# Performance work log

Hardware: AMD Instinct MI355X
Metric: run time of the kernel (lower is better)

Reference implementation:

```python
import jax, jax.numpy as jnp
import numpy as np

SIGMA = 1.0  # RBF kernel bandwidth (init kwarg)

def setup_inputs() -> dict:
    key = jax.random.key(0)
    ks = jax.random.split(key, 5)
    B, N, D_in, D_emb = 8, 2048, 1024, 512
    scale = 1.0 / np.sqrt(D_in)
    return {
        "x": jax.random.normal(ks[0], (B, N, D_in), jnp.float32),
        "W_mu": jax.random.normal(ks[1], (D_emb, D_in), jnp.float32) * scale,
        "b_mu": jax.random.normal(ks[2], (D_emb,), jnp.float32) * scale,
        "W_logvar": jax.random.normal(ks[3], (D_emb, D_in), jnp.float32) * scale,
        "b_logvar": jax.random.normal(ks[4], (D_emb,), jnp.float32) * scale,
    }

def reference(x, W_mu, b_mu, W_logvar, b_logvar):
    # dual linear heads: (B,N,D_in) -> (B,N,D_emb)
    mu = jnp.einsum('bnd,ed->bne', x, W_mu) + b_mu
    logvar = jnp.einsum('bnd,ed->bne', x, W_logvar) + b_logvar
    sigma = jnp.exp(0.5 * logvar)
    # RBF kernel matrix K(x, x): (B,N,N) via ||xi||^2 + ||xj||^2 - 2 xi.xj
    sq = jnp.sum(x * x, axis=-1)                       # (B,N)
    gram = jnp.einsum('bnd,bmd->bnm', x, x)            # (B,N,N)
    dist = sq[:, :, None] + sq[:, None, :] - 2.0 * gram
    K = jnp.exp(-dist / (2.0 * SIGMA ** 2))            # (B,N,N)
    cov_diag = jnp.diagonal(K, axis1=1, axis2=2)       # (B,N) == exp(0) = 1
    sigma_adjusted = sigma * cov_diag[..., None]       # (B,N,D_emb)
    return (mu, sigma_adjusted)
```

## Files before the change

kernel.cpp:

```cpp
#include <hip/hip_runtime.h>
#include <hip/hip_bf16.h>
#include <math.h>

typedef __bf16 bf16;
typedef __attribute__((ext_vector_type(4))) float f32x4;
typedef __attribute__((ext_vector_type(4))) bf16 bf16x4;
typedef __attribute__((ext_vector_type(8))) bf16 bf16x8;

#define M_TOT 16384
#define K_TOT 1024
#define D_EMB 512
#define NT 32

__global__ __launch_bounds__(256) void cvt_w_img(
    const float* __restrict__ W_mu, const float* __restrict__ W_logvar,
    bf16* __restrict__ img)
{
    const int c  = blockIdx.x * 256 + threadIdx.x;
    const int l  = c & 63;
    const int kt = (c >> 6) & 31;
    const int es = c >> 11;
    const int col = es * 16 + (l & 15);
    const int k0  = kt * 32 + (l >> 4) * 8;
    const float* s = (col < D_EMB) ? (W_mu + (size_t)col * K_TOT + k0)
                                   : (W_logvar + (size_t)(col - D_EMB) * K_TOT + k0);
    f32x4 a = ((const f32x4*)s)[0];
    f32x4 b = ((const f32x4*)s)[1];
    bf16x8 o;
    o[0] = (bf16)a[0]; o[1] = (bf16)a[1]; o[2] = (bf16)a[2]; o[3] = (bf16)a[3];
    o[4] = (bf16)b[0]; o[5] = (bf16)b[1]; o[6] = (bf16)b[2]; o[7] = (bf16)b[3];
    *(bf16x8*)(img + (size_t)c * 8) = o;
}

__global__ __launch_bounds__(512, 1) void gpe_tall(
    const float* __restrict__ x,
    const bf16* __restrict__ wimg,
    const float* __restrict__ b_mu,
    const float* __restrict__ b_logvar,
    float* __restrict__ out)
{
    __shared__ __align__(16) bf16 Alds[2][64 * 32];

    const int tid  = threadIdx.x;
    const int lane = tid & 63;
    const int wc   = tid >> 6;
    const int fr   = lane & 15;
    const int g16  = lane >> 4;
    const int bm   = blockIdx.x;

    const int arow = tid >> 3;
    const int aslot = tid & 7;
    const float* __restrict__ Asrc = x + (size_t)(bm * 64 + arow) * K_TOT + aslot * 4;
    const int awoff = arow * 32 + aslot * 4;

    const bf16* __restrict__ bb = wimg + (size_t)(wc * 8) * (NT * 512) + lane * 8;

    f32x4 acc[4][8];
#pragma unroll
    for (int m = 0; m < 4; ++m)
#pragma unroll
        for (int n = 0; n < 8; ++n)
            acc[m][n] = (f32x4){0.f, 0.f, 0.f, 0.f};

    f32x4  pfA;
    bf16x8 bvA[8], bvB[8];

    auto gloadA = [&](int t) { pfA = *(const f32x4*)(Asrc + t * 32); };
    auto cwA = [&](bf16* base) {
        bf16x4 w;
#pragma unroll
        for (int j = 0; j < 4; ++j) w[j] = (bf16)pfA[j];
        *(bf16x4*)&base[awoff] = w;
    };
    auto loadB = [&](int t, bf16x8 (&bv)[8]) {
#pragma unroll
        for (int ns = 0; ns < 8; ++ns)
            bv[ns] = *(const bf16x8*)(bb + (size_t)ns * (NT * 512) + t * 512);
    };

    gloadA(0);
    cwA(&Alds[0][0]);
    gloadA(1);
    loadB(0, bvA);
    asm volatile("s_waitcnt lgkmcnt(0)" ::: "memory");
    __builtin_amdgcn_s_barrier();

#define TILE_BODY(T, P, BVC, BVN)                                              \
    {                                                                          \
        const int t = (T);                                                     \
        if (t + 1 < NT) loadB(t + 1, BVN);                \
        bf16x8 afc[4];                                                         \
        _Pragma("unroll")                                                      \
        for (int m = 0; m < 4; ++m)                                            \
            afc[m] = *(const bf16x8*)&Alds[P][(m * 16 + fr) * 32 + g16 * 8];   \
        if (t + 1 < NT) {                                                      \
            cwA(&Alds[(P) ^ 1][0]);                   \
            if (t + 2 < NT) gloadA(t + 2);                                     \
        }                                                                      \
        __builtin_amdgcn_s_setprio(1);                                         \
        _Pragma("unroll")                                                      \
        for (int ns = 0; ns < 8; ++ns)                                         \
            _Pragma("unroll")                                                  \
            for (int m = 0; m < 4; ++m)                                        \
                acc[m][ns] = __builtin_amdgcn_mfma_f32_16x16x32_bf16(          \
                    afc[m], BVC[ns], acc[m][ns], 0, 0, 0);                     \
        __builtin_amdgcn_s_setprio(0);                                         \
        asm volatile("s_waitcnt lgkmcnt(0)" ::: "memory");                     \
        __builtin_amdgcn_s_barrier();                                          \
    }

    for (int t0 = 0; t0 < NT; t0 += 2) {
        TILE_BODY(t0,     0, bvA, bvB)
        TILE_BODY(t0 + 1, 1, bvB, bvA)
    }
#undef TILE_BODY

    const bool is_mu = (wc < 4);
    const float* __restrict__ bias = is_mu ? b_mu : b_logvar;
    float* __restrict__ obase = is_mu ? out : (out + (size_t)M_TOT * D_EMB);
    const int clbase = (wc & 3) * 128;

#pragma unroll
    for (int m = 0; m < 4; ++m) {
        const int row0 = bm * 64 + m * 16 + g16 * 4;
#pragma unroll
        for (int ns = 0; ns < 8; ++ns) {
            const int cl = clbase + ns * 16 + fr;
            const float bvs = bias[cl];
#pragma unroll
            for (int j = 0; j < 4; ++j) {
                float v = acc[m][ns][j] + bvs;
                if (!is_mu) v = __expf(0.5f * v);
                obase[(size_t)(row0 + j) * D_EMB + cl] = v;
            }
        }
    }
}

#define LDS_STRIDE 40
__global__ __launch_bounds__(256) void gpe_gemm_fb(
    const float* __restrict__ x, const float* __restrict__ W_mu,
    const float* __restrict__ b_mu, const float* __restrict__ W_logvar,
    const float* __restrict__ b_logvar, float* __restrict__ out)
{
    __shared__ __align__(16) bf16 As[128][LDS_STRIDE];
    __shared__ __align__(16) bf16 Bs[128][LDS_STRIDE];
    const int tid = threadIdx.x, lane = tid & 63, wid = tid >> 6;
    const int wr = wid >> 1, wcn = wid & 1;
    const int bn = blockIdx.x & 7, bm = blockIdx.x >> 3;
    const int ebase = bn * 128;
    const bool is_mu = (ebase < D_EMB);
    const float* Wp = is_mu ? (W_mu + (size_t)ebase * K_TOT)
                            : (W_logvar + (size_t)(ebase - D_EMB) * K_TOT);
    const float* bias = is_mu ? b_mu : b_logvar;
    const int cbase = is_mu ? ebase : (ebase - D_EMB);
    float* obase = is_mu ? out : (out + (size_t)M_TOT * D_EMB);
    const float* Ap = x + (size_t)(bm * 128) * K_TOT;
    f32x4 acc[4][4];
#pragma unroll
    for (int m = 0; m < 4; ++m)
#pragma unroll
        for (int n = 0; n < 4; ++n) acc[m][n] = (f32x4){0.f, 0.f, 0.f, 0.f};
    const int fr = lane & 15, fk = (lane >> 4) * 8;
    const int arow = wr * 64 + fr, brow = wcn * 64 + fr;
    for (int kt = 0; kt < K_TOT / 32; ++kt) {
        const int k0 = kt * 32;
#pragma unroll
        for (int s = 0; s < 4; ++s) {
            const int idx = s * 256 + tid;
            const int row = idx >> 3, col = (idx & 7) << 2;
            f32x4 va = *reinterpret_cast<const f32x4*>(Ap + (size_t)row * K_TOT + k0 + col);
            f32x4 vb = *reinterpret_cast<const f32x4*>(Wp + (size_t)row * K_TOT + k0 + col);
            bf16x4 ha, hb;
#pragma unroll
            for (int j = 0; j < 4; ++j) { ha[j] = (bf16)va[j]; hb[j] = (bf16)vb[j]; }
            *reinterpret_cast<bf16x4*>(&As[row][col]) = ha;
            *reinterpret_cast<bf16x4*>(&Bs[row][col]) = hb;
        }
        __syncthreads();
        bf16x8 af[4], bfv[4];
#pragma unroll
        for (int m = 0; m < 4; ++m)
            af[m] = *reinterpret_cast<const bf16x8*>(&As[arow + m * 16][fk]);
#pragma unroll
        for (int n = 0; n < 4; ++n)
            bfv[n] = *reinterpret_cast<const bf16x8*>(&Bs[brow + n * 16][fk]);
#pragma unroll
        for (int m = 0; m < 4; ++m)
#pragma unroll
            for (int n = 0; n < 4; ++n)
                acc[m][n] = __builtin_amdgcn_mfma_f32_16x16x32_bf16(af[m], bfv[n], acc[m][n], 0, 0, 0);
        __syncthreads();
    }
#pragma unroll
    for (int m = 0; m < 4; ++m) {
        const int rbase = bm * 128 + wr * 64 + m * 16 + (lane >> 4) * 4;
#pragma unroll
        for (int n = 0; n < 4; ++n) {
            const int c = cbase + wcn * 64 + n * 16 + (lane & 15);
            const float bv = bias[c];
#pragma unroll
            for (int j = 0; j < 4; ++j) {
                float v = acc[m][n][j] + bv;
                if (!is_mu) v = __expf(0.5f * v);
                obase[(size_t)(rbase + j) * D_EMB + c] = v;
            }
        }
    }
}

extern "C" void kernel_launch(void* const* d_in, const int* in_sizes, int n_in,
                              void* d_out, int out_size, void* d_ws, size_t ws_size,
                              hipStream_t stream) {
    const float* x        = (const float*)d_in[0];
    const float* W_mu     = (const float*)d_in[1];
    const float* b_mu     = (const float*)d_in[2];
    const float* W_logvar = (const float*)d_in[3];
    const float* b_logvar = (const float*)d_in[4];
    float* out = (float*)d_out;

    const size_t ws_needed = (size_t)1024 * 1024 * sizeof(bf16);

    if (ws_size >= ws_needed) {
        bf16* wimg = (bf16*)d_ws;
        cvt_w_img<<<512, 256, 0, stream>>>(W_mu, W_logvar, wimg);
        gpe_tall<<<256, 512, 0, stream>>>(x, wimg, b_mu, b_logvar, out);
    } else {
        gpe_gemm_fb<<<1024, 256, 0, stream>>>(x, W_mu, b_mu, W_logvar, b_logvar, out);
    }
}
```

Before: 54.86 us.

## Stage full A row-panel in LDS once and drop per-tile barriers

Instead of double-buffering 64x32 A tiles with a barrier every k-step, each block loads and converts its entire 64x1024 A panel into LDS up front, using an XOR swizzle to avoid bank conflicts. The main loop then runs with no barriers, and B fragments are prefetched two tiles ahead into the register buffer that was just consumed. This removes per-tile synchronisation and conversion work from the MFMA loop. The cost is 128KB of LDS per block and an unoverlapped prologue that loads all of A before any compute starts.

```diff
diff --git a/kernel.cpp b/kernel.cpp
--- a/kernel.cpp
+++ b/kernel.cpp
@@ -32,71 +32,68 @@
     *(bf16x8*)(img + (size_t)c * 8) = o;
 }
 
-__global__ __launch_bounds__(512, 1) void gpe_tall(
+__global__ __launch_bounds__(512, 1) void gpe_tall2(
     const float* __restrict__ x,
     const bf16* __restrict__ wimg,
     const float* __restrict__ b_mu,
     const float* __restrict__ b_logvar,
     float* __restrict__ out)
 {
-    __shared__ __align__(16) bf16 Alds[2][64 * 32];
+    __shared__ __align__(16) bf16 Alds[64 * 1024];
 
     const int tid  = threadIdx.x;
     const int lane = tid & 63;
     const int wc   = tid >> 6;
     const int fr   = lane & 15;
     const int g16  = lane >> 4;
+    const int frx  = fr & 7;
     const int bm   = blockIdx.x;
 
-    const int arow = tid >> 3;
-    const int aslot = tid & 7;
-    const float* __restrict__ Asrc = x + (size_t)(bm * 64 + arow) * K_TOT + aslot * 4;
-    const int awoff = arow * 32 + aslot * 4;
-
     const bf16* __restrict__ bb = wimg + (size_t)(wc * 8) * (NT * 512) + lane * 8;
 
-    f32x4 acc[4][8];
-#pragma unroll
-    for (int m = 0; m < 4; ++m)
-#pragma unroll
-        for (int n = 0; n < 8; ++n)
-            acc[m][n] = (f32x4){0.f, 0.f, 0.f, 0.f};
-
-    f32x4  pfA;
     bf16x8 bvA[8], bvB[8];
-
-    auto gloadA = [&](int t) { pfA = *(const f32x4*)(Asrc + t * 32); };
-    auto cwA = [&](bf16* base) {
-        bf16x4 w;
-#pragma unroll
-        for (int j = 0; j < 4; ++j) w[j] = (bf16)pfA[j];
-        *(bf16x4*)&base[awoff] = w;
-    };
     auto loadB = [&](int t, bf16x8 (&bv)[8]) {
 #pragma unroll
         for (int ns = 0; ns < 8; ++ns)
             bv[ns] = *(const bf16x8*)(bb + (size_t)ns * (NT * 512) + t * 512);
     };
 
-    gloadA(0);
-    cwA(&Alds[0][0]);
-    gloadA(1);
     loadB(0, bvA);
-    asm volatile("s_waitcnt lgkmcnt(0)" ::: "memory");
-    __builtin_amdgcn_s_barrier();
-
-#define TILE_BODY(T, P, BVC, BVN)                                              \
+    loadB(1, bvB);
+
+    {
+        const int arow = tid >> 3;
+        const int sl0  = tid & 7;
+        const float* __restrict__ Asrc = x + (size_t)(bm * 64 + arow) * K_TOT;
+        const int rx = arow & 7;
+#pragma unroll
+        for (int j = 0; j < 16; ++j) {
+            const int slot = sl0 + 8 * j;
+            f32x4 a = *(const f32x4*)(Asrc + slot * 8);
+            f32x4 b = *(const f32x4*)(Asrc + slot * 8 + 4);
+            bf16x8 w;
+#pragma unroll
+            for (int q = 0; q < 4; ++q) { w[q] = (bf16)a[q]; w[q + 4] = (bf16)b[q]; }
+            *(bf16x8*)&Alds[arow * 1024 + (slot ^ rx) * 8] = w;
+        }
+    }
+    __syncthreads();
+
+    f32x4 acc[4][8];
+#pragma unroll
+    for (int m = 0; m < 4; ++m)
+#pragma unroll
+        for (int n = 0; n < 8; ++n)
+            acc[m][n] = (f32x4){0.f, 0.f, 0.f, 0.f};
+
+#define TILE_BODY(T, BVC)                                                      \
     {                                                                          \
         const int t = (T);                                                     \
-        if (t + 1 < NT) loadB(t + 1, BVN);                \
         bf16x8 afc[4];                                                         \
         _Pragma("unroll")                                                      \
         for (int m = 0; m < 4; ++m)                                            \
-            afc[m] = *(const bf16x8*)&Alds[P][(m * 16 + fr) * 32 + g16 * 8];   \
-        if (t + 1 < NT) {                                                      \
-            cwA(&Alds[(P) ^ 1][0]);                   \
-            if (t + 2 < NT) gloadA(t + 2);                                     \
-        }                                                                      \
+            afc[m] = *(const bf16x8*)&Alds[(m * 16 + fr) * 1024                \
+                                           + ((t * 4 + g16) ^ frx) * 8];       \
         __builtin_amdgcn_s_setprio(1);                                         \
         _Pragma("unroll")                                                      \
         for (int ns = 0; ns < 8; ++ns)                                         \
@@ -105,13 +102,12 @@
                 acc[m][ns] = __builtin_amdgcn_mfma_f32_16x16x32_bf16(          \
                     afc[m], BVC[ns], acc[m][ns], 0, 0, 0);                     \
         __builtin_amdgcn_s_setprio(0);                                         \
-        asm volatile("s_waitcnt lgkmcnt(0)" ::: "memory");                     \
-        __builtin_amdgcn_s_barrier();                                          \
+        if (t + 2 < NT) loadB(t + 2, BVC);     \
     }
 
     for (int t0 = 0; t0 < NT; t0 += 2) {
-        TILE_BODY(t0,     0, bvA, bvB)
-        TILE_BODY(t0 + 1, 1, bvB, bvA)
+        TILE_BODY(t0,     bvA)
+        TILE_BODY(t0 + 1, bvB)
     }
 #undef TILE_BODY
 
@@ -224,7 +220,7 @@
     if (ws_size >= ws_needed) {
         bf16* wimg = (bf16*)d_ws;
         cvt_w_img<<<512, 256, 0, stream>>>(W_mu, W_logvar, wimg);
-        gpe_tall<<<256, 512, 0, stream>>>(x, wimg, b_mu, b_logvar, out);
+        gpe_tall2<<<256, 512, 0, stream>>>(x, wimg, b_mu, b_logvar, out);
     } else {
         gpe_gemm_fb<<<1024, 256, 0, stream>>>(x, W_mu, b_mu, W_logvar, b_logvar, out);
     }
```

New measurement: 53.72 us. 1.02x faster.
